# Optimization experiments

Measured on AMD Instinct MI355X. Metric: run time of the kernel, lower is better.

The kernel has to match this reference:

```python
import jax, jax.numpy as jnp
import numpy as np
import math


def _dct2_mat(N):
    # DCT-II matrix, norm=None convention of torch_dct: X[k] = 2*sum_n x[n]*cos(pi*(2n+1)*k/(2N))
    n = np.arange(N)
    k = n[:, None]
    C = 2.0 * np.cos(np.pi * (2 * n[None, :] + 1) * k / (2 * N))
    return jnp.asarray(C, dtype=jnp.float32)


def setup_inputs() -> dict:
    key = jax.random.key(0)
    k1, k2, k3 = jax.random.split(key, 3)
    B, H, W = 128, 256, 256
    thresh = int(H / (2 * math.sqrt(2)))  # 90
    x = jax.random.normal(k1, (B, 3, H, W), dtype=jnp.float32)
    w = jax.random.normal(k2, (1, thresh), dtype=jnp.float32) * 0.05
    b = jax.random.normal(k3, (1,), dtype=jnp.float32) * 0.05
    return {"x": x, "w": w, "b": b}


def reference(x, w, b):
    B, C, H, W = x.shape
    Ch = _dct2_mat(H)
    Cw = _dct2_mat(W)
    # dct_2d: DCT-II along last two dims
    xd = jnp.einsum('bchw,kw->bchk', x, Cw)
    xd = jnp.einsum('bchk,jh->bcjk', xd, Ch)
    xd = jax.lax.stop_gradient(xd)  # original does x.detach() inside get_fft_feature
    gray = 0.2989 * xd[:, 0] + 0.587 * xd[:, 1] + 0.114 * xd[:, 2]  # [B,H,W]
    F = jnp.fft.fft2(gray, axes=(-2, -1))
    re = F.real + 1e-8  # original adds epsilon to both real and imag parts
    im = F.imag + 1e-8
    mag = jnp.log(jnp.sqrt(re * re + im * im + 1e-10) + 1e-10)
    mag = jnp.fft.fftshift(mag, axes=(-2, -1))  # quadrant-swap `shift` == fftshift for even dims
    # radial binning (static integer radii, as in azimuthalAverage)
    yy, xx = np.indices([H, W])
    r = np.sqrt((xx - H / 2) ** 2 + (yy - W / 2) ** 2).astype(np.int32).ravel()
    nbins = int(r.max()) + 1
    nr = jnp.asarray(np.bincount(r, minlength=nbins).astype(np.float32))
    rj = jnp.asarray(r)
    tbin = jax.vmap(lambda m: jax.ops.segment_sum(m, rj, num_segments=nbins))(mag.reshape(B, -1))
    prof = tbin / (nr + 1e-10)  # [B, nbins]
    prof = prof[:, 1:-2]  # azimuthalAverage returns radial_prof[1:-2]
    mn = jnp.min(prof, axis=1, keepdims=True)
    mx = jnp.max(prof, axis=1, keepdims=True)
    out = (prof - mn) / (mx - mn)
    out = jnp.where(jnp.isnan(out), 0.0, out)
    thresh = w.shape[1]
    feat = out[:, -thresh:]  # [B, thresh]
    return feat @ w.T + b  # [B, 1]
```

## Files before the change

### kernel.cpp

```cpp
#include <hip/hip_runtime.h>
#include <math.h>

#define NBINS 182
#define NB 128

typedef unsigned short u16;
typedef __attribute__((ext_vector_type(8))) short short8;
typedef __attribute__((ext_vector_type(4))) float f32x4;

__device__ __forceinline__ u16 f2bf(float f) {
    union { float f; unsigned u; } v; v.f = f;
    unsigned r = v.u + 0x7FFF + ((v.u >> 16) & 1);
    return (u16)(r >> 16);
}
__device__ __forceinline__ float bf2f(u16 u) {
    union { unsigned u; float f; } v; v.u = ((unsigned)u) << 16;
    return v.f;
}
__device__ __forceinline__ short8 negbf(short8 v) {
    short8 r;
#pragma unroll
    for (int i = 0; i < 8; ++i) r[i] = v[i] ^ (short)0x8000;
    return r;
}

__device__ __forceinline__ int radial_bin(int dx, int dy) {
    int d2 = dx * dx + dy * dy;
    int bin = (int)sqrtf((float)d2);
    while ((bin + 1) * (bin + 1) <= d2) ++bin;
    while (bin * bin > d2) --bin;
    return bin;
}

__global__ __launch_bounds__(256) void prep(float* __restrict__ M_re,
                                            float* __restrict__ M_im,
                                            u16* __restrict__ A1,
                                            float* __restrict__ nrpart,
                                            float* __restrict__ tbin,
                                            u16* __restrict__ Tt_im,
                                            unsigned* __restrict__ done) {
    __shared__ double ctab[1024];
    __shared__ double stab[1024];
    __shared__ float s[NBINS];
    int blk = blockIdx.x;
    int t = threadIdx.x;

    if (blk < 256) {
        for (int i = t; i < 1024; i += 256) {
            double a = 3.14159265358979323846 * (double)i / 512.0;
            ctab[i] = cos(a);
            stab[i] = sin(a);
        }
        __syncthreads();
        int j = blk;
        int w = t;
        double re = 0.0, im = 0.0;
        int tw = 2 * w + 1;
        for (int k = 0; k < 256; ++k) {
            int e = (4 * j * k) & 1023;
            int m = (tw * k) & 1023;
            double cw = 2.0 * ctab[m];
            re += ctab[e] * cw;
            im -= stab[e] * cw;
        }
        M_re[j * 256 + w] = (float)re;
        M_im[j * 256 + w] = (float)im;
        A1[j * 256 + w] = f2bf((float)re);
        A1[(j + 256) * 256 + w] = f2bf((float)im);
    } else if (blk < 512) {
        int i = blk - 256;
        if (t < NBINS) s[t] = 0.0f;
        __syncthreads();
        int bin = radial_bin(t - 128, i - 128);
        atomicAdd(&s[bin], 1.0f);
        __syncthreads();
        if (t < NBINS) nrpart[i * NBINS + t] = s[t];
    } else {
        int idx = (blk - 512) * 256 + t;
        for (int i = idx; i < NB * NBINS; i += 8192) tbin[i] = 0.0f;
        for (int i = idx; i < NB * 128; i += 8192) {
            int bb = i >> 7, off = (i & 127) << 1;
            *(unsigned*)(Tt_im + (size_t)bb * 65536 + 128 * 256 + off) = 0u;
        }
        if (idx < NB) done[idx] = 0u;
    }
}

__global__ __launch_bounds__(512) void s1(const u16* __restrict__ A1,
                                          const float* __restrict__ x,
                                          u16* __restrict__ Tt_re,
                                          u16* __restrict__ Tt_im) {
    __shared__ u16 As[272 * 40];
    __shared__ u16 Bs[128 * 40];
    int b = blockIdx.z;
    int h0 = blockIdx.x * 128;
    int t = threadIdx.x;
    int lane = t & 63, wv = t >> 6;
    int w4 = wv & 3;
    int wr = (w4 >> 1) * 64;
    int wc = (w4 & 1) * 64;
    int aOff = (wv >= 4) ? 128 : 0;
    int fr = lane & 15;
    int fk = (lane >> 4) << 3;

    f32x4 acc[4][4];
#pragma unroll
    for (int i = 0; i < 4; ++i)
#pragma unroll
        for (int j = 0; j < 4; ++j) acc[i][j] = (f32x4){0.f, 0.f, 0.f, 0.f};
    f32x4 acc128 = (f32x4){0.f, 0.f, 0.f, 0.f};

    int srow = t >> 2, swq = (t & 3) << 3;
    const float* xp = x + (size_t)b * 196608 + (size_t)(h0 + srow) * 256 + swq;

    for (int kk = 0; kk < 256; kk += 32) {
        for (int c = t; c < 1088; c += 512) {
            int row = c >> 2, off = (c & 3) << 3;
            int src = (row < 128) ? row : ((row < 256) ? row + 128 : row - 128);
            *(uint4*)&As[row * 40 + off] =
                *(const uint4*)(A1 + (size_t)src * 256 + kk + off);
        }
        {
            const float* p = xp + kk;
            float4 ra = *(const float4*)p;
            float4 rb = *(const float4*)(p + 4);
            float4 ga = *(const float4*)(p + 65536);
            float4 gb = *(const float4*)(p + 65540);
            float4 ba = *(const float4*)(p + 131072);
            float4 bb = *(const float4*)(p + 131076);
            float q0 = 0.2989f * ra.x + 0.587f * ga.x + 0.114f * ba.x;
            float q1 = 0.2989f * ra.y + 0.587f * ga.y + 0.114f * ba.y;
            float q2 = 0.2989f * ra.z + 0.587f * ga.z + 0.114f * ba.z;
            float q3 = 0.2989f * ra.w + 0.587f * ga.w + 0.114f * ba.w;
            float q4 = 0.2989f * rb.x + 0.587f * gb.x + 0.114f * bb.x;
            float q5 = 0.2989f * rb.y + 0.587f * gb.y + 0.114f * bb.y;
            float q6 = 0.2989f * rb.z + 0.587f * gb.z + 0.114f * bb.z;
            float q7 = 0.2989f * rb.w + 0.587f * gb.w + 0.114f * bb.w;
            uint4 o;
            o.x = (unsigned)f2bf(q0) | ((unsigned)f2bf(q1) << 16);
            o.y = (unsigned)f2bf(q2) | ((unsigned)f2bf(q3) << 16);
            o.z = (unsigned)f2bf(q4) | ((unsigned)f2bf(q5) << 16);
            o.w = (unsigned)f2bf(q6) | ((unsigned)f2bf(q7) << 16);
            *(uint4*)&Bs[srow * 40 + swq] = o;
        }
        __syncthreads();
        short8 af[4], bfr[4];
#pragma unroll
        for (int i = 0; i < 4; ++i)
            af[i] = *(const short8*)&As[(aOff + wr + i * 16 + fr) * 40 + fk];
#pragma unroll
        for (int j = 0; j < 4; ++j)
            bfr[j] = *(const short8*)&Bs[(wc + j * 16 + fr) * 40 + fk];
#pragma unroll
        for (int i = 0; i < 4; ++i)
#pragma unroll
            for (int j = 0; j < 4; ++j)
                acc[i][j] = __builtin_amdgcn_mfma_f32_16x16x32_bf16(
                    af[i], bfr[j], acc[i][j], 0, 0, 0);
        {
            short8 a128 = *(const short8*)&As[(256 + fr) * 40 + fk];
            short8 b128 = *(const short8*)&Bs[(wv * 16 + fr) * 40 + fk];
            acc128 = __builtin_amdgcn_mfma_f32_16x16x32_bf16(
                a128, b128, acc128, 0, 0, 0);
        }
        __syncthreads();
    }

    u16* dst = ((wv < 4) ? Tt_re : Tt_im) + (size_t)b * 65536;
    int rq = (lane >> 4) << 2;
#pragma unroll
    for (int i = 0; i < 4; ++i)
#pragma unroll
        for (int j = 0; j < 4; ++j) {
            int col = h0 + wc + j * 16 + fr;
#pragma unroll
            for (int reg = 0; reg < 4; ++reg) {
                int row = wr + i * 16 + rq + reg;
                dst[(size_t)row * 256 + col] = f2bf(acc[i][j][reg]);
            }
        }
    if ((lane >> 4) == 0)
        Tt_re[(size_t)b * 65536 + 128 * 256 + h0 + wv * 16 + fr] = f2bf(acc128[0]);
}

__global__ __launch_bounds__(256) void s2f(const u16* __restrict__ A1,
                                           const float* __restrict__ M_re,
                                           const u16* __restrict__ Tt_re,
                                           const u16* __restrict__ Tt_im,
                                           float* __restrict__ tbin,
                                           const float* __restrict__ nrpart,
                                           const float* __restrict__ wgt,
                                           const float* __restrict__ bias,
                                           float* __restrict__ out,
                                           unsigned* __restrict__ done) {
    __shared__ u16 Ar[64 * 40], Ai[64 * 40], Br[64 * 40], Bi[64 * 40];
    __shared__ float sbins[NBINS];
    __shared__ float sM[256];
    __shared__ float prof[NBINS];
    __shared__ float smn, smx, ssum;
    __shared__ int sOld;
    int blk = blockIdx.x;
    int t = threadIdx.x;
    int b;

    if (blk >= 1024) {
        b = blk - 1024;
        sM[t] = M_re[128 * 256 + t];
        __syncthreads();
        if (t <= 128) {
            const u16* pr = Tt_re + (size_t)b * 65536 + (size_t)t * 256;
            const u16* pi = Tt_im + (size_t)b * 65536 + (size_t)t * 256;
            float re = 0.0f, im = 0.0f;
            for (int h = 0; h < 256; h += 8) {
                uint4 vr = *(const uint4*)(pr + h);
                uint4 vi = *(const uint4*)(pi + h);
                unsigned wr[4] = {vr.x, vr.y, vr.z, vr.w};
                unsigned wi[4] = {vi.x, vi.y, vi.z, vi.w};
#pragma unroll
                for (int q = 0; q < 4; ++q) {
                    re = fmaf(sM[h + 2 * q], bf2f((u16)(wr[q] & 0xffff)), re);
                    re = fmaf(sM[h + 2 * q + 1], bf2f((u16)(wr[q] >> 16)), re);
                    im = fmaf(sM[h + 2 * q], bf2f((u16)(wi[q] & 0xffff)), im);
                    im = fmaf(sM[h + 2 * q + 1], bf2f((u16)(wi[q] >> 16)), im);
                }
            }
            re += 1e-8f; im += 1e-8f;
            float mag = logf(sqrtf(re * re + im * im + 1e-10f) + 1e-10f);
            float wj = (t == 0 || t == 128) ? 1.0f : 2.0f;
            int dx = (t < 128) ? t : t - 256;
            int bin = radial_bin(dx, -128);
            atomicAdd(&tbin[b * NBINS + bin], wj * mag);
        }
    } else {
        b = blk >> 3;
        int u0 = ((blk >> 2) & 1) * 64;
        int j0 = (blk & 3) * 64;
        int lane = t & 63, wv = t >> 6;
        int wu = (wv >> 1) * 32;
        int wj = (wv & 1) * 32;
        int fr = lane & 15;
        int fk = (lane >> 4) << 3;

        for (int i = t; i < NBINS; i += 256) sbins[i] = 0.0f;

        f32x4 accr[2][2], acci[2][2];
#pragma unroll
        for (int i = 0; i < 2; ++i)
#pragma unroll
            for (int j = 0; j < 2; ++j) {
                accr[i][j] = (f32x4){0.f, 0.f, 0.f, 0.f};
                acci[i][j] = (f32x4){0.f, 0.f, 0.f, 0.f};
            }

        const u16* Apr = A1 + (size_t)u0 * 256;
        const u16* Api = A1 + (size_t)(256 + u0) * 256;

        int lrow = t >> 2, loff = (t & 3) << 3;
        int jp = j0 + lrow;
        int src = (jp <= 128) ? jp : 256 - jp;
        unsigned imask = (jp > 128) ? 0x80008000u : 0u;
        const u16* Trs = Tt_re + (size_t)b * 65536 + (size_t)src * 256;
        const u16* Tis = Tt_im + (size_t)b * 65536 + (size_t)src * 256;

        for (int kk = 0; kk < 256; kk += 32) {
            *(uint4*)&Ar[lrow * 40 + loff] =
                *(const uint4*)(Apr + (size_t)lrow * 256 + kk + loff);
            *(uint4*)&Ai[lrow * 40 + loff] =
                *(const uint4*)(Api + (size_t)lrow * 256 + kk + loff);
            *(uint4*)&Br[lrow * 40 + loff] = *(const uint4*)(Trs + kk + loff);
            uint4 vi = *(const uint4*)(Tis + kk + loff);
            vi.x ^= imask; vi.y ^= imask; vi.z ^= imask; vi.w ^= imask;
            *(uint4*)&Bi[lrow * 40 + loff] = vi;
            __syncthreads();
            short8 arf[2], aif[2], naif[2], brf[2], bif[2];
#pragma unroll
            for (int i = 0; i < 2; ++i) {
                arf[i] = *(const short8*)&Ar[(wu + i * 16 + fr) * 40 + fk];
                aif[i] = *(const short8*)&Ai[(wu + i * 16 + fr) * 40 + fk];
                naif[i] = negbf(aif[i]);
            }
#pragma unroll
            for (int j = 0; j < 2; ++j) {
                brf[j] = *(const short8*)&Br[(wj + j * 16 + fr) * 40 + fk];
                bif[j] = *(const short8*)&Bi[(wj + j * 16 + fr) * 40 + fk];
            }
#pragma unroll
            for (int i = 0; i < 2; ++i)
#pragma unroll
                for (int j = 0; j < 2; ++j) {
                    accr[i][j] = __builtin_amdgcn_mfma_f32_16x16x32_bf16(
                        arf[i], brf[j], accr[i][j], 0, 0, 0);
                    accr[i][j] = __builtin_amdgcn_mfma_f32_16x16x32_bf16(
                        naif[i], bif[j], accr[i][j], 0, 0, 0);
                    acci[i][j] = __builtin_amdgcn_mfma_f32_16x16x32_bf16(
                        arf[i], bif[j], acci[i][j], 0, 0, 0);
                    acci[i][j] = __builtin_amdgcn_mfma_f32_16x16x32_bf16(
                        aif[i], brf[j], acci[i][j], 0, 0, 0);
                }
            __syncthreads();
        }

        int rq = (lane >> 4) << 2;
#pragma unroll
        for (int i = 0; i < 2; ++i)
#pragma unroll
            for (int j = 0; j < 2; ++j) {
                int v = j0 + wj + j * 16 + fr;
                int dx = (v < 128) ? v : v - 256;
#pragma unroll
                for (int reg = 0; reg < 4; ++reg) {
                    int u = u0 + wu + i * 16 + rq + reg;
                    float wrow = (u == 0) ? 1.0f : 2.0f;
                    int bin = radial_bin(dx, u);
                    float re = accr[i][j][reg] + 1e-8f;
                    float im = acci[i][j][reg] + 1e-8f;
                    float mag = logf(sqrtf(re * re + im * im + 1e-10f) + 1e-10f);
                    atomicAdd(&sbins[bin], wrow * mag);
                }
            }
        __syncthreads();
        for (int i = t; i < NBINS; i += 256)
            atomicAdd(&tbin[b * NBINS + i], sbins[i]);
    }

    __syncthreads();
    if (t == 0) {
        __threadfence();
        sOld = (int)atomicAdd(&done[b], 1u);
    }
    __syncthreads();
    if (sOld == 8) {
        if (t < NBINS) {
            float nr = 0.0f;
            for (int i = 0; i < 256; ++i) nr += nrpart[i * NBINS + t];
            float tb = atomicAdd(&tbin[b * NBINS + t], 0.0f);
            prof[t] = tb / (nr + 1e-10f);
        }
        __syncthreads();
        if (t == 0) {
            float mn = prof[1], mx = prof[1];
            for (int i = 2; i <= 179; ++i) {
                float p = prof[i];
                mn = fminf(mn, p);
                mx = fmaxf(mx, p);
            }
            smn = mn; smx = mx; ssum = 0.0f;
        }
        __syncthreads();
        if (t < 90) {
            float denom = smx - smn;
            float v = (prof[90 + t] - smn) / denom;
            if (v != v) v = 0.0f;
            atomicAdd(&ssum, v * wgt[t]);
        }
        __syncthreads();
        if (t == 0) out[b] = ssum + bias[0];
    }
}

extern "C" void kernel_launch(void* const* d_in, const int* in_sizes, int n_in,
                              void* d_out, int out_size, void* d_ws, size_t ws_size,
                              hipStream_t stream) {
    const float* x = (const float*)d_in[0];
    const float* w = (const float*)d_in[1];
    const float* bias = (const float*)d_in[2];
    float* out = (float*)d_out;

    float* M_re = (float*)d_ws;
    float* M_im = M_re + 65536;
    u16* A1 = (u16*)(M_im + 65536);
    u16* Tt_re = A1 + 131072;
    u16* Tt_im = Tt_re + (size_t)NB * 65536;
    float* tbin = (float*)(Tt_im + (size_t)NB * 65536);
    float* nrpart = tbin + NB * NBINS;
    unsigned* done = (unsigned*)(nrpart + 256 * NBINS);

    prep<<<544, 256, 0, stream>>>(M_re, M_im, A1, nrpart, tbin, Tt_im, done);
    s1<<<dim3(2, 1, NB), 512, 0, stream>>>(A1, x, Tt_re, Tt_im);
    s2f<<<1152, 256, 0, stream>>>(A1, M_re, Tt_re, Tt_im, tbin,
                                  nrpart, w, bias, out, done);
}
```

Before: 241.4 us.

## Split s1 into smaller 256-thread blocks and move finalization to separate kernel

```diff
diff --git a/kernel.cpp b/kernel.cpp
--- a/kernel.cpp
+++ b/kernel.cpp
@@ -37,8 +37,7 @@
                                             u16* __restrict__ A1,
                                             float* __restrict__ nrpart,
                                             float* __restrict__ tbin,
-                                            u16* __restrict__ Tt_im,
-                                            unsigned* __restrict__ done) {
+                                            u16* __restrict__ Tt_im) {
     __shared__ double ctab[1024];
     __shared__ double stab[1024];
     __shared__ float s[NBINS];
@@ -82,24 +81,22 @@
             int bb = i >> 7, off = (i & 127) << 1;
             *(unsigned*)(Tt_im + (size_t)bb * 65536 + 128 * 256 + off) = 0u;
         }
-        if (idx < NB) done[idx] = 0u;
-    }
-}
-
-__global__ __launch_bounds__(512) void s1(const u16* __restrict__ A1,
+    }
+}
+
+__global__ __launch_bounds__(256) void s1(const u16* __restrict__ A1,
                                           const float* __restrict__ x,
                                           u16* __restrict__ Tt_re,
                                           u16* __restrict__ Tt_im) {
     __shared__ u16 As[272 * 40];
-    __shared__ u16 Bs[128 * 40];
+    __shared__ u16 Bs[64 * 40];
     int b = blockIdx.z;
-    int h0 = blockIdx.x * 128;
+    int h0 = blockIdx.x * 64;
     int t = threadIdx.x;
     int lane = t & 63, wv = t >> 6;
-    int w4 = wv & 3;
-    int wr = (w4 >> 1) * 64;
-    int wc = (w4 & 1) * 64;
-    int aOff = (wv >= 4) ? 128 : 0;
+    int isIm = wv >> 1;
+    int rhalf = (wv & 1) * 64;
+    int aOff = isIm ? 128 : 0;
     int fr = lane & 15;
     int fk = (lane >> 4) << 3;
 
@@ -114,7 +111,7 @@
     const float* xp = x + (size_t)b * 196608 + (size_t)(h0 + srow) * 256 + swq;
 
     for (int kk = 0; kk < 256; kk += 32) {
-        for (int c = t; c < 1088; c += 512) {
+        for (int c = t; c < 1088; c += 256) {
             int row = c >> 2, off = (c & 3) << 3;
             int src = (row < 128) ? row : ((row < 256) ? row + 128 : row - 128);
             *(uint4*)&As[row * 40 + off] =
@@ -147,10 +144,10 @@
         short8 af[4], bfr[4];
 #pragma unroll
         for (int i = 0; i < 4; ++i)
-            af[i] = *(const short8*)&As[(aOff + wr + i * 16 + fr) * 40 + fk];
+            af[i] = *(const short8*)&As[(aOff + rhalf + i * 16 + fr) * 40 + fk];
 #pragma unroll
         for (int j = 0; j < 4; ++j)
-            bfr[j] = *(const short8*)&Bs[(wc + j * 16 + fr) * 40 + fk];
+            bfr[j] = *(const short8*)&Bs[(j * 16 + fr) * 40 + fk];
 #pragma unroll
         for (int i = 0; i < 4; ++i)
 #pragma unroll
@@ -166,16 +163,16 @@
         __syncthreads();
     }
 
-    u16* dst = ((wv < 4) ? Tt_re : Tt_im) + (size_t)b * 65536;
+    u16* dst = (isIm ? Tt_im : Tt_re) + (size_t)b * 65536;
     int rq = (lane >> 4) << 2;
 #pragma unroll
     for (int i = 0; i < 4; ++i)
 #pragma unroll
         for (int j = 0; j < 4; ++j) {
-            int col = h0 + wc + j * 16 + fr;
+            int col = h0 + j * 16 + fr;
 #pragma unroll
             for (int reg = 0; reg < 4; ++reg) {
-                int row = wr + i * 16 + rq + reg;
+                int row = rhalf + i * 16 + rq + reg;
                 dst[(size_t)row * 256 + col] = f2bf(acc[i][j][reg]);
             }
         }
@@ -187,175 +184,167 @@
                                            const float* __restrict__ M_re,
                                            const u16* __restrict__ Tt_re,
                                            const u16* __restrict__ Tt_im,
-                                           float* __restrict__ tbin,
-                                           const float* __restrict__ nrpart,
-                                           const float* __restrict__ wgt,
-                                           const float* __restrict__ bias,
-                                           float* __restrict__ out,
-                                           unsigned* __restrict__ done) {
+                                           float* __restrict__ tbin) {
     __shared__ u16 Ar[64 * 40], Ai[64 * 40], Br[64 * 40], Bi[64 * 40];
     __shared__ float sbins[NBINS];
     __shared__ float sM[256];
+    int blk = blockIdx.x;
+    int t = threadIdx.x;
+
+    if (blk >= 1024) {
+        int b = blk - 1024;
+        sM[t] = M_re[128 * 256 + t];
+        __syncthreads();
+        if (t > 128) return;
+        const u16* pr = Tt_re + (size_t)b * 65536 + (size_t)t * 256;
+        const u16* pi = Tt_im + (size_t)b * 65536 + (size_t)t * 256;
+        float re = 0.0f, im = 0.0f;
+        for (int h = 0; h < 256; h += 8) {
+            uint4 vr = *(const uint4*)(pr + h);
+            uint4 vi = *(const uint4*)(pi + h);
+            unsigned wr[4] = {vr.x, vr.y, vr.z, vr.w};
+            unsigned wi[4] = {vi.x, vi.y, vi.z, vi.w};
+#pragma unroll
+            for (int q = 0; q < 4; ++q) {
+                re = fmaf(sM[h + 2 * q], bf2f((u16)(wr[q] & 0xffff)), re);
+                re = fmaf(sM[h + 2 * q + 1], bf2f((u16)(wr[q] >> 16)), re);
+                im = fmaf(sM[h + 2 * q], bf2f((u16)(wi[q] & 0xffff)), im);
+                im = fmaf(sM[h + 2 * q + 1], bf2f((u16)(wi[q] >> 16)), im);
+            }
+        }
+        re += 1e-8f; im += 1e-8f;
+        float mag = logf(sqrtf(re * re + im * im + 1e-10f) + 1e-10f);
+        float wj = (t == 0 || t == 128) ? 1.0f : 2.0f;
+        int dx = (t < 128) ? t : t - 256;
+        int bin = radial_bin(dx, -128);
+        atomicAdd(&tbin[b * NBINS + bin], wj * mag);
+        return;
+    }
+
+    int b = blk >> 3;
+    int u0 = ((blk >> 2) & 1) * 64;
+    int j0 = (blk & 3) * 64;
+    int lane = t & 63, wv = t >> 6;
+    int wu = (wv >> 1) * 32;
+    int wj = (wv & 1) * 32;
+    int fr = lane & 15;
+    int fk = (lane >> 4) << 3;
+
+    for (int i = t; i < NBINS; i += 256) sbins[i] = 0.0f;
+
+    f32x4 accr[2][2], acci[2][2];
+#pragma unroll
+    for (int i = 0; i < 2; ++i)
+#pragma unroll
+        for (int j = 0; j < 2; ++j) {
+            accr[i][j] = (f32x4){0.f, 0.f, 0.f, 0.f};
+            acci[i][j] = (f32x4){0.f, 0.f, 0.f, 0.f};
+        }
+
+    const u16* Apr = A1 + (size_t)u0 * 256;
+    const u16* Api = A1 + (size_t)(256 + u0) * 256;
+
+    int lrow = t >> 2, loff = (t & 3) << 3;
+    int jp = j0 + lrow;
+    int src = (jp <= 128) ? jp : 256 - jp;
+    unsigned imask = (jp > 128) ? 0x80008000u : 0u;
+    const u16* Trs = Tt_re + (size_t)b * 65536 + (size_t)src * 256;
+    const u16* Tis = Tt_im + (size_t)b * 65536 + (size_t)src * 256;
+
+    for (int kk = 0; kk < 256; kk += 32) {
+        *(uint4*)&Ar[lrow * 40 + loff] =
+            *(const uint4*)(Apr + (size_t)lrow * 256 + kk + loff);
+        *(uint4*)&Ai[lrow * 40 + loff] =
+            *(const uint4*)(Api + (size_t)lrow * 256 + kk + loff);
+        *(uint4*)&Br[lrow * 40 + loff] = *(const uint4*)(Trs + kk + loff);
+        uint4 vi = *(const uint4*)(Tis + kk + loff);
+        vi.x ^= imask; vi.y ^= imask; vi.z ^= imask; vi.w ^= imask;
+        *(uint4*)&Bi[lrow * 40 + loff] = vi;
+        __syncthreads();
+        short8 arf[2], aif[2], naif[2], brf[2], bif[2];
+#pragma unroll
+        for (int i = 0; i < 2; ++i) {
+            arf[i] = *(const short8*)&Ar[(wu + i * 16 + fr) * 40 + fk];
+            aif[i] = *(const short8*)&Ai[(wu + i * 16 + fr) * 40 + fk];
+            naif[i] = negbf(aif[i]);
+        }
+#pragma unroll
+        for (int j = 0; j < 2; ++j) {
+            brf[j] = *(const short8*)&Br[(wj + j * 16 + fr) * 40 + fk];
+            bif[j] = *(const short8*)&Bi[(wj + j * 16 + fr) * 40 + fk];
+        }
+#pragma unroll
+        for (int i = 0; i < 2; ++i)
+#pragma unroll
+            for (int j = 0; j < 2; ++j) {
+                accr[i][j] = __builtin_amdgcn_mfma_f32_16x16x32_bf16(
+                    arf[i], brf[j], accr[i][j], 0, 0, 0);
+                accr[i][j] = __builtin_amdgcn_mfma_f32_16x16x32_bf16(
+                    naif[i], bif[j], accr[i][j], 0, 0, 0);
+                acci[i][j] = __builtin_amdgcn_mfma_f32_16x16x32_bf16(
+                    arf[i], bif[j], acci[i][j], 0, 0, 0);
+                acci[i][j] = __builtin_amdgcn_mfma_f32_16x16x32_bf16(
+                    aif[i], brf[j], acci[i][j], 0, 0, 0);
+            }
+        __syncthreads();
+    }
+
+    int rq = (lane >> 4) << 2;
+#pragma unroll
+    for (int i = 0; i < 2; ++i)
+#pragma unroll
+        for (int j = 0; j < 2; ++j) {
+            int v = j0 + wj + j * 16 + fr;
+            int dx = (v < 128) ? v : v - 256;
+#pragma unroll
+            for (int reg = 0; reg < 4; ++reg) {
+                int u = u0 + wu + i * 16 + rq + reg;
+                float wrow = (u == 0) ? 1.0f : 2.0f;
+                int bin = radial_bin(dx, u);
+                float re = accr[i][j][reg] + 1e-8f;
+                float im = acci[i][j][reg] + 1e-8f;
+                float mag = logf(sqrtf(re * re + im * im + 1e-10f) + 1e-10f);
+                atomicAdd(&sbins[bin], wrow * mag);
+            }
+        }
+    __syncthreads();
+    for (int i = t; i < NBINS; i += 256)
+        atomicAdd(&tbin[b * NBINS + i], sbins[i]);
+}
+
+__global__ __launch_bounds__(192) void finalize(const float* __restrict__ tbin,
+                                                const float* __restrict__ nrpart,
+                                                const float* __restrict__ w,
+                                                const float* __restrict__ bias,
+                                                float* __restrict__ out) {
     __shared__ float prof[NBINS];
     __shared__ float smn, smx, ssum;
-    __shared__ int sOld;
-    int blk = blockIdx.x;
+    int b = blockIdx.x;
     int t = threadIdx.x;
-    int b;
-
-    if (blk >= 1024) {
-        b = blk - 1024;
-        sM[t] = M_re[128 * 256 + t];
-        __syncthreads();
-        if (t <= 128) {
-            const u16* pr = Tt_re + (size_t)b * 65536 + (size_t)t * 256;
-            const u16* pi = Tt_im + (size_t)b * 65536 + (size_t)t * 256;
-            float re = 0.0f, im = 0.0f;
-            for (int h = 0; h < 256; h += 8) {
-                uint4 vr = *(const uint4*)(pr + h);
-                uint4 vi = *(const uint4*)(pi + h);
-                unsigned wr[4] = {vr.x, vr.y, vr.z, vr.w};
-                unsigned wi[4] = {vi.x, vi.y, vi.z, vi.w};
-#pragma unroll
-                for (int q = 0; q < 4; ++q) {
-                    re = fmaf(sM[h + 2 * q], bf2f((u16)(wr[q] & 0xffff)), re);
-                    re = fmaf(sM[h + 2 * q + 1], bf2f((u16)(wr[q] >> 16)), re);
-                    im = fmaf(sM[h + 2 * q], bf2f((u16)(wi[q] & 0xffff)), im);
-                    im = fmaf(sM[h + 2 * q + 1], bf2f((u16)(wi[q] >> 16)), im);
-                }
-            }
-            re += 1e-8f; im += 1e-8f;
-            float mag = logf(sqrtf(re * re + im * im + 1e-10f) + 1e-10f);
-            float wj = (t == 0 || t == 128) ? 1.0f : 2.0f;
-            int dx = (t < 128) ? t : t - 256;
-            int bin = radial_bin(dx, -128);
-            atomicAdd(&tbin[b * NBINS + bin], wj * mag);
-        }
-    } else {
-        b = blk >> 3;
-        int u0 = ((blk >> 2) & 1) * 64;
-        int j0 = (blk & 3) * 64;
-        int lane = t & 63, wv = t >> 6;
-        int wu = (wv >> 1) * 32;
-        int wj = (wv & 1) * 32;
-        int fr = lane & 15;
-        int fk = (lane >> 4) << 3;
-
-        for (int i = t; i < NBINS; i += 256) sbins[i] = 0.0f;
-
-        f32x4 accr[2][2], acci[2][2];
-#pragma unroll
-        for (int i = 0; i < 2; ++i)
-#pragma unroll
-            for (int j = 0; j < 2; ++j) {
-                accr[i][j] = (f32x4){0.f, 0.f, 0.f, 0.f};
-                acci[i][j] = (f32x4){0.f, 0.f, 0.f, 0.f};
-            }
-
-        const u16* Apr = A1 + (size_t)u0 * 256;
-        const u16* Api = A1 + (size_t)(256 + u0) * 256;
-
-        int lrow = t >> 2, loff = (t & 3) << 3;
-        int jp = j0 + lrow;
-        int src = (jp <= 128) ? jp : 256 - jp;
-        unsigned imask = (jp > 128) ? 0x80008000u : 0u;
-        const u16* Trs = Tt_re + (size_t)b * 65536 + (size_t)src * 256;
-        const u16* Tis = Tt_im + (size_t)b * 65536 + (size_t)src * 256;
-
-        for (int kk = 0; kk < 256; kk += 32) {
-            *(uint4*)&Ar[lrow * 40 + loff] =
-                *(const uint4*)(Apr + (size_t)lrow * 256 + kk + loff);
-            *(uint4*)&Ai[lrow * 40 + loff] =
-                *(const uint4*)(Api + (size_t)lrow * 256 + kk + loff);
-            *(uint4*)&Br[lrow * 40 + loff] = *(const uint4*)(Trs + kk + loff);
-            uint4 vi = *(const uint4*)(Tis + kk + loff);
-            vi.x ^= imask; vi.y ^= imask; vi.z ^= imask; vi.w ^= imask;
-            *(uint4*)&Bi[lrow * 40 + loff] = vi;
-            __syncthreads();
-            short8 arf[2], aif[2], naif[2], brf[2], bif[2];
-#pragma unroll
-            for (int i = 0; i < 2; ++i) {
-                arf[i] = *(const short8*)&Ar[(wu + i * 16 + fr) * 40 + fk];
-                aif[i] = *(const short8*)&Ai[(wu + i * 16 + fr) * 40 + fk];
-                naif[i] = negbf(aif[i]);
-            }
-#pragma unroll
-            for (int j = 0; j < 2; ++j) {
-                brf[j] = *(const short8*)&Br[(wj + j * 16 + fr) * 40 + fk];
-                bif[j] = *(const short8*)&Bi[(wj + j * 16 + fr) * 40 + fk];
-            }
-#pragma unroll
-            for (int i = 0; i < 2; ++i)
-#pragma unroll
-                for (int j = 0; j < 2; ++j) {
-                    accr[i][j] = __builtin_amdgcn_mfma_f32_16x16x32_bf16(
-                        arf[i], brf[j], accr[i][j], 0, 0, 0);
-                    accr[i][j] = __builtin_amdgcn_mfma_f32_16x16x32_bf16(
-                        naif[i], bif[j], accr[i][j], 0, 0, 0);
-                    acci[i][j] = __builtin_amdgcn_mfma_f32_16x16x32_bf16(
-                        arf[i], bif[j], acci[i][j], 0, 0, 0);
-                    acci[i][j] = __builtin_amdgcn_mfma_f32_16x16x32_bf16(
-                        aif[i], brf[j], acci[i][j], 0, 0, 0);
-                }
-            __syncthreads();
-        }
-
-        int rq = (lane >> 4) << 2;
-#pragma unroll
-        for (int i = 0; i < 2; ++i)
-#pragma unroll
-            for (int j = 0; j < 2; ++j) {
-                int v = j0 + wj + j * 16 + fr;
-                int dx = (v < 128) ? v : v - 256;
-#pragma unroll
-                for (int reg = 0; reg < 4; ++reg) {
-                    int u = u0 + wu + i * 16 + rq + reg;
-                    float wrow = (u == 0) ? 1.0f : 2.0f;
-                    int bin = radial_bin(dx, u);
-                    float re = accr[i][j][reg] + 1e-8f;
-                    float im = acci[i][j][reg] + 1e-8f;
-                    float mag = logf(sqrtf(re * re + im * im + 1e-10f) + 1e-10f);
-                    atomicAdd(&sbins[bin], wrow * mag);
-                }
-            }
-        __syncthreads();
-        for (int i = t; i < NBINS; i += 256)
-            atomicAdd(&tbin[b * NBINS + i], sbins[i]);
-    }
-
+    if (t < NBINS) {
+        float nr = 0.0f;
+        for (int i = 0; i < 256; ++i) nr += nrpart[i * NBINS + t];
+        prof[t] = tbin[b * NBINS + t] / (nr + 1e-10f);
+    }
     __syncthreads();
     if (t == 0) {
-        __threadfence();
-        sOld = (int)atomicAdd(&done[b], 1u);
+        float mn = prof[1], mx = prof[1];
+        for (int i = 2; i <= 179; ++i) {
+            float p = prof[i];
+            mn = fminf(mn, p);
+            mx = fmaxf(mx, p);
+        }
+        smn = mn; smx = mx; ssum = 0.0f;
     }
     __syncthreads();
-    if (sOld == 8) {
-        if (t < NBINS) {
-            float nr = 0.0f;
-            for (int i = 0; i < 256; ++i) nr += nrpart[i * NBINS + t];
-            float tb = atomicAdd(&tbin[b * NBINS + t], 0.0f);
-            prof[t] = tb / (nr + 1e-10f);
-        }
-        __syncthreads();
-        if (t == 0) {
-            float mn = prof[1], mx = prof[1];
-            for (int i = 2; i <= 179; ++i) {
-                float p = prof[i];
-                mn = fminf(mn, p);
-                mx = fmaxf(mx, p);
-            }
-            smn = mn; smx = mx; ssum = 0.0f;
-        }
-        __syncthreads();
-        if (t < 90) {
-            float denom = smx - smn;
-            float v = (prof[90 + t] - smn) / denom;
-            if (v != v) v = 0.0f;
-            atomicAdd(&ssum, v * wgt[t]);
-        }
-        __syncthreads();
-        if (t == 0) out[b] = ssum + bias[0];
-    }
+    if (t < 90) {
+        float denom = smx - smn;
+        float v = (prof[90 + t] - smn) / denom;
+        if (v != v) v = 0.0f;
+        atomicAdd(&ssum, v * w[t]);
+    }
+    __syncthreads();
+    if (t == 0) out[b] = ssum + bias[0];
 }
 
 extern "C" void kernel_launch(void* const* d_in, const int* in_sizes, int n_in,
@@ -373,10 +362,9 @@
     u16* Tt_im = Tt_re + (size_t)NB * 65536;
     float* tbin = (float*)(Tt_im + (size_t)NB * 65536);
     float* nrpart = tbin + NB * NBINS;
-    unsigned* done = (unsigned*)(nrpart + 256 * NBINS);
-
-    prep<<<544, 256, 0, stream>>>(M_re, M_im, A1, nrpart, tbin, Tt_im, done);
-    s1<<<dim3(2, 1, NB), 512, 0, stream>>>(A1, x, Tt_re, Tt_im);
-    s2f<<<1152, 256, 0, stream>>>(A1, M_re, Tt_re, Tt_im, tbin,
-                                  nrpart, w, bias, out, done);
-}
+
+    prep<<<544, 256, 0, stream>>>(M_re, M_im, A1, nrpart, tbin, Tt_im);
+    s1<<<dim3(4, 1, NB), 256, 0, stream>>>(A1, x, Tt_re, Tt_im);
+    s2f<<<1152, 256, 0, stream>>>(A1, M_re, Tt_re, Tt_im, tbin);
+    finalize<<<NB, 192, 0, stream>>>(tbin, nrpart, w, bias, out);
+}
```

Result: faster. 232.3 us (-3.8%).
